# Optimization experiments

Measured on AMD Instinct MI355X. Metric: run time of the kernel, lower is better.

## Reference

```python
import jax, jax.numpy as jnp
import numpy as np

L, B, T, D = 4, 2, 1024, 2048
HQ, HKV, DK = 16, 4, 128
HID = 5464
CAND = 896


def setup_inputs() -> dict:
    key = jax.random.key(0)
    ks = jax.random.split(key, 8)
    s = lambda fan: fan ** -0.5
    return {
        "x": jax.random.normal(ks[0], (B, T, D), jnp.float32),
        "s1": jnp.ones((L, D), jnp.float32),
        "s2": jnp.ones((L, D), jnp.float32),
        "s3": jnp.ones((L, D), jnp.float32),
        "wq": jax.random.normal(ks[1], (L, D, HQ * DK), jnp.float32) * s(D),
        "wk": jax.random.normal(ks[2], (L, D, HKV * DK), jnp.float32) * s(D),
        "wv": jax.random.normal(ks[3], (L, D, HKV * DK), jnp.float32) * s(D),
        "wo": jax.random.normal(ks[4], (L, HQ * DK, D), jnp.float32) * s(HQ * DK),
        "w_gate": jax.random.normal(ks[5], (L, D, HID), jnp.float32) * s(D),
        "w_val": jax.random.normal(ks[6], (L, D, HID), jnp.float32) * s(D),
        "w_out": jax.random.normal(ks[7], (L, HID, D), jnp.float32) * s(HID),
        "cand_offset": CAND,
    }


def _rmsnorm(x, scale, eps=1e-5):
    xf = x.astype(jnp.float32)
    n = xf * jax.lax.rsqrt(jnp.mean(xf * xf, axis=-1, keepdims=True) + eps)
    return (scale * n).astype(x.dtype)


def _rope_cos_sin(t_len, dk):
    inv = 1.0 / (10000.0 ** (jnp.arange(0, dk, 2, dtype=jnp.float32) / dk))
    fr = jnp.outer(jnp.arange(t_len, dtype=jnp.float32), inv)
    emb = jnp.concatenate([fr, fr], axis=-1)  # [T, dk]
    return jnp.cos(emb)[None, :, None, :], jnp.sin(emb)[None, :, None, :]


def _rotate_half(x):
    x1, x2 = jnp.split(x, 2, axis=-1)
    return jnp.concatenate([-x2, x1], axis=-1)


def reference(x, s1, s2, s3, wq, wk, wv, wo, w_gate, w_val, w_out, cand_offset):
    Bsz, Tlen, _ = x.shape
    # recsys mask: causal history; candidates attend to history + self only
    r = jnp.arange(Tlen)[:, None]
    c = jnp.arange(Tlen)[None, :]
    mask = (c <= r) & ~((r >= cand_offset) & (c >= cand_offset) & (r != c))  # [T,T] bool
    cos, sin = _rope_cos_sin(Tlen, DK)
    nrep = HQ // HKV
    h = x
    for l in range(wq.shape[0]):
        hn = _rmsnorm(h, s1[l])
        q = (hn @ wq[l]).reshape(Bsz, Tlen, HQ, DK)
        k = (hn @ wk[l]).reshape(Bsz, Tlen, HKV, DK)
        v = (hn @ wv[l]).reshape(Bsz, Tlen, HKV, DK)
        q = q * cos + _rotate_half(q) * sin
        k = k * cos + _rotate_half(k) * sin
        k = jnp.repeat(k, nrep, axis=2)  # GQA expand -> [B,T,HQ,DK]
        v = jnp.repeat(v, nrep, axis=2)
        logits = jnp.einsum('bthd,bshd->bhts', q, k)  # attn_output_multiplier = 1.0
        logits = jnp.where(mask[None, None], logits, -jnp.inf)
        attn = jax.nn.softmax(logits.astype(jnp.float32), axis=-1).astype(x.dtype)
        o = jnp.einsum('bhts,bshd->bthd', attn, v).reshape(Bsz, Tlen, HQ * DK)
        h = h + o @ wo[l]
        hn = _rmsnorm(h, s2[l])
        ff = (jax.nn.gelu(hn @ w_gate[l], approximate=False) * (hn @ w_val[l])) @ w_out[l]
        h = h + ff
        h = _rmsnorm(h, s3[l])
    return h
```

## Files before the change

### kernel.cpp

```cpp
#include <hip/hip_runtime.h>
#include <stdint.h>

#define L_ 4
#define B_ 2
#define T_ 1024
#define D_ 2048
#define HQ_ 16
#define HKV_ 4
#define DK_ 128
#define HID_ 5464
#define HIDP_ 5504
#define BT_ (B_*T_)

typedef unsigned short u16;
typedef float f32x4 __attribute__((ext_vector_type(4)));
typedef __bf16 bf16x8 __attribute__((ext_vector_type(8)));

__device__ __forceinline__ u16 f2bs(float f) {
  unsigned u = __float_as_uint(f);
  u += 0x7fffu + ((u >> 16) & 1u);
  return (u16)(u >> 16);
}
__device__ __forceinline__ float bs2f(u16 s) {
  return __uint_as_float(((unsigned)s) << 16);
}

__device__ __forceinline__ void async16(void* lds, const void* g) {
  __builtin_amdgcn_global_load_lds(
      (const __attribute__((address_space(1))) unsigned*)(uintptr_t)g,
      (__attribute__((address_space(3))) unsigned*)(unsigned)(uintptr_t)lds,
      16, 0, 0);
}

__device__ __forceinline__ f32x4 mfma16(bf16x8 a, bf16x8 b, f32x4 c) {
  return __builtin_amdgcn_mfma_f32_16x16x32_bf16(a, b, c, 0, 0, 0);
}

__device__ __forceinline__ void remap_bid(int& bm, int& bn) {
  const int nbx = gridDim.x, nby = gridDim.y;
  const int nwg = nbx * nby;
  const int lin = blockIdx.y * nbx + blockIdx.x;
  const int q = nwg >> 3, r = nwg & 7;
  const int xcd = lin & 7, rest = lin >> 3;
  const int wgid = (xcd < r ? xcd * (q + 1) : r * (q + 1) + (xcd - r) * q) + rest;
  const int GROUP = 4;
  const int tpg = GROUP * nby;
  const int gid = wgid / tpg;
  const int first = gid * GROUP;
  const int size = (GROUP < nbx - first) ? GROUP : (nbx - first);
  const int rem = wgid - gid * tpg;
  bn = first + rem % size;
  bm = rem / size;
}

__global__ void copy_f4_k(const float4* __restrict__ src, float4* __restrict__ dst, int n4) {
  int i = blockIdx.x * blockDim.x + threadIdx.x;
  if (i < n4) dst[i] = src[i];
}

__global__ void rope_tab_k(float* __restrict__ ct, float* __restrict__ st) {
  int idx = blockIdx.x * 256 + threadIdx.x;
  int t = idx >> 6, i = idx & 63;
  float inv = expf(-(float)i * (9.210340371976184f / 64.f));
  float fr = (float)t * inv;
  ct[idx] = cosf(fr);
  st[idx] = sinf(fr);
}

__global__ __launch_bounds__(256) void cvt_split_k(const float4* __restrict__ in,
    uint2* __restrict__ ohi, uint2* __restrict__ olo, int n4) {
  int i = blockIdx.x * 256 + threadIdx.x;
  if (i >= n4) return;
  float4 v = in[i];
  u16 h0 = f2bs(v.x), h1 = f2bs(v.y), h2 = f2bs(v.z), h3 = f2bs(v.w);
  u16 l0 = f2bs(v.x - bs2f(h0)), l1 = f2bs(v.y - bs2f(h1));
  u16 l2 = f2bs(v.z - bs2f(h2)), l3 = f2bs(v.w - bs2f(h3));
  uint2 ph, pl;
  ph.x = (unsigned)h0 | ((unsigned)h1 << 16); ph.y = (unsigned)h2 | ((unsigned)h3 << 16);
  pl.x = (unsigned)l0 | ((unsigned)l1 << 16); pl.y = (unsigned)l2 | ((unsigned)l3 << 16);
  ohi[i] = ph; olo[i] = pl;
}

__global__ __launch_bounds__(256) void transpose_split_k(
    const float* __restrict__ in, u16* __restrict__ outh, u16* __restrict__ outl,
    int inR, int inC, int outC) {
  __shared__ float tile[64][65];
  const int oj0 = blockIdx.x * 64;
  const int oi0 = blockIdx.y * 64;
  #pragma unroll
  for (int rep = 0; rep < 16; ++rep) {
    int idx = rep * 256 + threadIdx.x;
    int a = idx >> 6, b = idx & 63;
    int ir = oj0 + a, ic = oi0 + b;
    tile[a][b] = (ir < inR && ic < inC) ? in[(size_t)ir * inC + ic] : 0.f;
  }
  __syncthreads();
  #pragma unroll
  for (int rep = 0; rep < 16; ++rep) {
    int idx = rep * 256 + threadIdx.x;
    int ii = idx >> 6, jj = idx & 63;
    float val = tile[jj][ii];
    u16 hh = f2bs(val);
    const size_t o = (size_t)(oi0 + ii) * outC + oj0 + jj;
    outh[o] = hh;
    outl[o] = f2bs(val - bs2f(hh));
  }
}

__global__ __launch_bounds__(256) void transpose_v_split_k(const float* __restrict__ v,
    u16* __restrict__ vth, u16* __restrict__ vtl) {
  __shared__ float tile[64][65];
  const int bz = blockIdx.z;
  const int b = bz >> 2, hkv = bz & 3;
  const int t0 = blockIdx.x * 64, d0 = blockIdx.y * 64;
  #pragma unroll
  for (int rep = 0; rep < 16; ++rep) {
    int idx = rep * 256 + threadIdx.x;
    int a = idx >> 6, c = idx & 63;
    tile[a][c] = v[((size_t)(b * T_ + t0 + a) * HKV_ + hkv) * DK_ + d0 + c];
  }
  __syncthreads();
  #pragma unroll
  for (int rep = 0; rep < 16; ++rep) {
    int idx = rep * 256 + threadIdx.x;
    int aa = idx & 63, cc = idx >> 6;
    float val = tile[aa][cc];
    u16 hh = f2bs(val);
    const size_t o = ((size_t)bz * DK_ + d0 + cc) * T_ + t0 + aa;
    vth[o] = hh;
    vtl[o] = f2bs(val - bs2f(hh));
  }
}

__global__ __launch_bounds__(256) void rmsnorm_f(const float* x,
    const float* __restrict__ sc, float* out) {
  const int row = blockIdx.x;
  const float* xr = x + (size_t)row * D_;
  float ss = 0.f;
  #pragma unroll
  for (int it = 0; it < D_ / 1024; ++it) {
    int i = (it * 256 + threadIdx.x) * 4;
    float4 v = *(const float4*)(xr + i);
    ss += v.x * v.x + v.y * v.y + v.z * v.z + v.w * v.w;
  }
  #pragma unroll
  for (int o = 1; o < 64; o <<= 1) ss += __shfl_xor(ss, o);
  __shared__ float red[4];
  if ((threadIdx.x & 63) == 0) red[threadIdx.x >> 6] = ss;
  __syncthreads();
  float tot = red[0] + red[1] + red[2] + red[3];
  float r = rsqrtf(tot * (1.f / D_) + 1e-5f);
  float* orow = out + (size_t)row * D_;
  #pragma unroll
  for (int it = 0; it < D_ / 1024; ++it) {
    int i = (it * 256 + threadIdx.x) * 4;
    float4 v = *(const float4*)(xr + i);
    float4 s4 = *(const float4*)(sc + i);
    float4 o4;
    o4.x = v.x * s4.x * r; o4.y = v.y * s4.y * r;
    o4.z = v.z * s4.z * r; o4.w = v.w * s4.w * r;
    *(float4*)(orow + i) = o4;
  }
}

__global__ __launch_bounds__(256) void rmsnorm_s(const float* x,
    const float* __restrict__ sc, u16* ohi, u16* olo) {
  const int row = blockIdx.x;
  const float* xr = x + (size_t)row * D_;
  float ss = 0.f;
  #pragma unroll
  for (int it = 0; it < D_ / 1024; ++it) {
    int i = (it * 256 + threadIdx.x) * 4;
    float4 v = *(const float4*)(xr + i);
    ss += v.x * v.x + v.y * v.y + v.z * v.z + v.w * v.w;
  }
  #pragma unroll
  for (int o = 1; o < 64; o <<= 1) ss += __shfl_xor(ss, o);
  __shared__ float red[4];
  if ((threadIdx.x & 63) == 0) red[threadIdx.x >> 6] = ss;
  __syncthreads();
  float tot = red[0] + red[1] + red[2] + red[3];
  float r = rsqrtf(tot * (1.f / D_) + 1e-5f);
  #pragma unroll
  for (int it = 0; it < D_ / 1024; ++it) {
    int i = (it * 256 + threadIdx.x) * 4;
    float4 v = *(const float4*)(xr + i);
    float4 s4 = *(const float4*)(sc + i);
    float o0 = v.x * s4.x * r, o1 = v.y * s4.y * r, o2 = v.z * s4.z * r, o3 = v.w * s4.w * r;
    u16 h0 = f2bs(o0), h1 = f2bs(o1), h2 = f2bs(o2), h3 = f2bs(o3);
    u16 l0 = f2bs(o0 - bs2f(h0)), l1 = f2bs(o1 - bs2f(h1));
    u16 l2 = f2bs(o2 - bs2f(h2)), l3 = f2bs(o3 - bs2f(h3));
    uint2 ph, pl;
    ph.x = (unsigned)h0 | ((unsigned)h1 << 16); ph.y = (unsigned)h2 | ((unsigned)h3 << 16);
    pl.x = (unsigned)l0 | ((unsigned)l1 << 16); pl.y = (unsigned)l2 | ((unsigned)l3 << 16);
    *(uint2*)(ohi + (size_t)row * D_ + i) = ph;
    *(uint2*)(olo + (size_t)row * D_ + i) = pl;
  }
}

template <int MODE>
__global__ __launch_bounds__(512, 4) void gemm_bts_k(
    const u16* __restrict__ Ahi, const u16* __restrict__ Alo,
    const u16* __restrict__ Bthi, const u16* __restrict__ Btlo,
    float* Cf, u16* Chi, u16* Clo, int N, int K) {
  __shared__ u16 smem[128 * 64 * 4];
  char* Ash = (char*)smem;
  char* Asl = (char*)smem + 16384;
  char* Bsh = (char*)smem + 32768;
  char* Bsl = (char*)smem + 49152;
  const int tid = threadIdx.x, w = tid >> 6, lane = tid & 63;
  const int g = lane >> 4, r16 = lane & 15;
  int bm, bn;
  remap_bid(bm, bn);
  const int m0 = bm * 128, n0 = bn * 128;
  const int wr = w >> 1, wc = w & 1;
  f32x4 acc[2][4] = {};
  const int nkt = K >> 6;
  for (int kt = 0; kt < nkt; ++kt) {
    #pragma unroll
    for (int inst = 0; inst < 2; ++inst) {
      const int p = (inst * 8 + w) * 1024 + lane * 16;
      const int row = p >> 7;
      const int sc = ((p >> 4) & 7) ^ (row & 7);
      const size_t ga = (size_t)(m0 + row) * K + (kt << 6) + sc * 8;
      const size_t gb = (size_t)(n0 + row) * K + (kt << 6) + sc * 8;
      async16(Ash + p, Ahi + ga);
      async16(Asl + p, Alo + ga);
      async16(Bsh + p, Bthi + gb);
      async16(Bsl + p, Btlo + gb);
    }
    asm volatile("s_waitcnt vmcnt(0)" ::: "memory");
    __syncthreads();
    #pragma unroll
    for (int ks = 0; ks < 2; ++ks) {
      bf16x8 ah[2], al[2], bh[4], bl[4];
      #pragma unroll
      for (int m = 0; m < 2; ++m) {
        const int row = wr * 32 + m * 16 + r16;
        const int ch = (ks * 4 + g) ^ (row & 7);
        const int off = row * 128 + ch * 16;
        ah[m] = *(const bf16x8*)(Ash + off);
        al[m] = *(const bf16x8*)(Asl + off);
      }
      #pragma unroll
      for (int n = 0; n < 4; ++n) {
        const int row = wc * 64 + n * 16 + r16;
        const int ch = (ks * 4 + g) ^ (row & 7);
        const int off = row * 128 + ch * 16;
        bh[n] = *(const bf16x8*)(Bsh + off);
        bl[n] = *(const bf16x8*)(Bsl + off);
      }
      #pragma unroll
      for (int m = 0; m < 2; ++m)
        #pragma unroll
        for (int n = 0; n < 4; ++n) {
          acc[m][n] = mfma16(ah[m], bh[n], acc[m][n]);
          acc[m][n] = mfma16(ah[m], bl[n], acc[m][n]);
          acc[m][n] = mfma16(al[m], bh[n], acc[m][n]);
        }
    }
    __syncthreads();
  }
  #pragma unroll
  for (int m = 0; m < 2; ++m) {
    const int rbase = m0 + wr * 32 + m * 16 + g * 4;
    #pragma unroll
    for (int n = 0; n < 4; ++n) {
      const int c = n0 + wc * 64 + n * 16 + r16;
      #pragma unroll
      for (int j = 0; j < 4; ++j) {
        const size_t idx = (size_t)(rbase + j) * N + c;
        const float v = acc[m][n][j];
        if constexpr (MODE == 0) {
          Cf[idx] = v;
        } else if constexpr (MODE == 1) {
          Cf[idx] += v;
        } else if constexpr (MODE == 2) {
          const float gv = bs2f(Chi[idx]) + bs2f(Clo[idx]);
          const float ge = 0.5f * gv * (1.f + erff(gv * 0.70710678118654752f));
          const float r = ge * v;
          const u16 rh = f2bs(r);
          Chi[idx] = rh;
          Clo[idx] = f2bs(r - bs2f(rh));
        } else {
          const u16 rh = f2bs(v);
          Chi[idx] = rh;
          Clo[idx] = f2bs(v - bs2f(rh));
        }
      }
    }
  }
}

__global__ __launch_bounds__(256) void rope_f_k(float* q, float* k,
    const float* __restrict__ ct, const float* __restrict__ st) {
  const int row = blockIdx.x;
  const int t = row & (T_ - 1);
  float* qr = q + (size_t)row * (HQ_ * DK_);
  for (int idx = threadIdx.x; idx < HQ_ * 64; idx += 256) {
    int h = idx >> 6, i = idx & 63;
    float c = ct[t * 64 + i], s = st[t * 64 + i];
    float x1 = qr[h * DK_ + i], x2 = qr[h * DK_ + i + 64];
    qr[h * DK_ + i]      = x1 * c - x2 * s;
    qr[h * DK_ + i + 64] = x2 * c + x1 * s;
  }
  float* kr = k + (size_t)row * (HKV_ * DK_);
  for (int idx = threadIdx.x; idx < HKV_ * 64; idx += 256) {
    int h = idx >> 6, i = idx & 63;
    float c = ct[t * 64 + i], s = st[t * 64 + i];
    float x1 = kr[h * DK_ + i], x2 = kr[h * DK_ + i + 64];
    kr[h * DK_ + i]      = x1 * c - x2 * s;
    kr[h * DK_ + i + 64] = x2 * c + x1 * s;
  }
}

__global__ __launch_bounds__(256) void attn_s_k(
    const u16* __restrict__ Qh, const u16* __restrict__ Ql,
    const u16* __restrict__ Kh, const u16* __restrict__ Kl,
    const u16* __restrict__ VTh, const u16* __restrict__ VTl,
    u16* __restrict__ Ohi, u16* __restrict__ Olo, const int* __restrict__ candp) {
  __shared__ u16 sm[40960];
  char* Kth = (char*)sm;
  char* Ktl = (char*)sm + 16384;
  char* Vth = (char*)sm + 32768;
  char* Vtl = (char*)sm + 49152;
  const int b = blockIdx.z, hq = blockIdx.y, q0 = blockIdx.x * 64;
  const int hkv = hq >> 2;
  const int tid = threadIdx.x, w = tid >> 6, lane = tid & 63;
  const int g = lane >> 4, r16 = lane & 15;
  char* Pth = (char*)sm + 65536 + w * 2048;
  char* Ptl = (char*)sm + 65536 + 8192 + w * 2048;
  const int CANDv = *candp;
  const int qrow = q0 + w * 16 + r16;
  const int pmask = (r16 & 7) << 4;
  const u16* qph = Qh + ((size_t)(b * T_ + qrow) * HQ_ + hq) * DK_;
  const u16* qpl = Ql + ((size_t)(b * T_ + qrow) * HQ_ + hq) * DK_;
  bf16x8 qh[4], ql[4];
  #pragma unroll
  for (int ks = 0; ks < 4; ++ks) {
    qh[ks] = *(const bf16x8*)(qph + ks * 32 + g * 8);
    ql[ks] = *(const bf16x8*)(qpl + ks * 32 + g * 8);
  }

  float m_run = -1e30f, l_run = 0.f;
  f32x4 oacc[8] = {};

  const int ntile = blockIdx.x + 1;
  for (int it = 0; it < ntile; ++it) {
    const int c0 = it * 64;
    if (c0 >= CANDv && c0 + 63 < q0) continue;
    #pragma unroll
    for (int inst = 0; inst < 4; ++inst) {
      const int p = (inst * 4 + w) * 1024 + lane * 16;
      const int rowK = p >> 8;
      const int scK = ((p >> 4) & 15) ^ (rowK & 7);
      const size_t gk = ((size_t)(b * T_ + c0 + rowK) * HKV_ + hkv) * DK_ + scK * 8;
      async16(Kth + p, Kh + gk);
      async16(Ktl + p, Kl + gk);
      const int rowV = p >> 7;
      const int scV = ((p >> 4) & 7) ^ (rowV & 7);
      const size_t gv = ((size_t)(b * HKV_ + hkv) * DK_ + rowV) * T_ + c0 + scV * 8;
      async16(Vth + p, VTh + gv);
      async16(Vtl + p, VTl + gv);
    }
    asm volatile("s_waitcnt vmcnt(0)" ::: "memory");
    __syncthreads();

    f32x4 stf[4] = {};
    #pragma unroll
    for (int ks = 0; ks < 4; ++ks) {
      #pragma unroll
      for (int kf = 0; kf < 4; ++kf) {
        const int row = kf * 16 + r16;
        const int ch = (ks * 4 + g) ^ (row & 7);
        const int off = row * 256 + ch * 16;
        bf16x8 akh = *(const bf16x8*)(Kth + off);
        bf16x8 akl = *(const bf16x8*)(Ktl + off);
        stf[kf] = mfma16(akh, qh[ks], stf[kf]);
        stf[kf] = mfma16(akh, ql[ks], stf[kf]);
        stf[kf] = mfma16(akl, qh[ks], stf[kf]);
      }
    }
    float pv[16];
    float tmax = -1e30f;
    #pragma unroll
    for (int kf = 0; kf < 4; ++kf)
      #pragma unroll
      for (int j = 0; j < 4; ++j) {
        const int c = c0 + kf * 16 + g * 4 + j;
        float s = stf[kf][j];
        const bool ok = (c <= qrow) && !((qrow >= CANDv) && (c >= CANDv) && (c != qrow));
        s = ok ? s : -1e30f;
        pv[kf * 4 + j] = s;
        tmax = fmaxf(tmax, s);
      }
    tmax = fmaxf(tmax, __shfl_xor(tmax, 16));
    tmax = fmaxf(tmax, __shfl_xor(tmax, 32));
    const float mnew = fmaxf(m_run, tmax);
    const float scal = __expf(m_run - mnew);
    float psum = 0.f;
    #pragma unroll
    for (int i = 0; i < 16; ++i) {
      const float e = (pv[i] > -1e29f) ? __expf(pv[i] - mnew) : 0.f;
      pv[i] = e; psum += e;
    }
    psum += __shfl_xor(psum, 16);
    psum += __shfl_xor(psum, 32);
    l_run = l_run * scal + psum;
    m_run = mnew;
    #pragma unroll
    for (int df = 0; df < 8; ++df)
      #pragma unroll
      for (int j = 0; j < 4; ++j) oacc[df][j] *= scal;
    #pragma unroll
    for (int kf = 0; kf < 4; ++kf) {
      u16 h0 = f2bs(pv[kf * 4 + 0]), h1 = f2bs(pv[kf * 4 + 1]);
      u16 h2 = f2bs(pv[kf * 4 + 2]), h3 = f2bs(pv[kf * 4 + 3]);
      u16 l0 = f2bs(pv[kf * 4 + 0] - bs2f(h0)), l1 = f2bs(pv[kf * 4 + 1] - bs2f(h1));
      u16 l2 = f2bs(pv[kf * 4 + 2] - bs2f(h2)), l3 = f2bs(pv[kf * 4 + 3] - bs2f(h3));
      uint2 ph, pl;
      ph.x = (unsigned)h0 | ((unsigned)h1 << 16); ph.y = (unsigned)h2 | ((unsigned)h3 << 16);
      pl.x = (unsigned)l0 | ((unsigned)l1 << 16); pl.y = (unsigned)l2 | ((unsigned)l3 << 16);
      *(uint2*)(Pth + r16 * 128 + ((kf * 32 + g * 8) ^ pmask)) = ph;
      *(uint2*)(Ptl + r16 * 128 + ((kf * 32 + g * 8) ^ pmask)) = pl;
    }
    asm volatile("s_waitcnt lgkmcnt(0)" ::: "memory");
    __builtin_amdgcn_sched_barrier(0);
    #pragma unroll
    for (int ks = 0; ks < 2; ++ks) {
      bf16x8 pfh = *(const bf16x8*)(Pth + r16 * 128 + ((ks * 64 + g * 16) ^ pmask));
      bf16x8 pfl = *(const bf16x8*)(Ptl + r16 * 128 + ((ks * 64 + g * 16) ^ pmask));
      #pragma unroll
      for (int df = 0; df < 8; ++df) {
        const int row = df * 16 + r16;
        const int ch = (ks * 4 + g) ^ (row & 7);
        const int off = row * 128 + ch * 16;
        bf16x8 avh = *(const bf16x8*)(Vth + off);
        bf16x8 avl = *(const bf16x8*)(Vtl + off);
        oacc[df] = mfma16(avh, pfh, oacc[df]);
        oacc[df] = mfma16(avh, pfl, oacc[df]);
        oacc[df] = mfma16(avl, pfh, oacc[df]);
      }
    }
    __syncthreads();
  }
  const float inv = 1.f / l_run;
  u16* oph = Ohi + ((size_t)(b * T_ + qrow) * HQ_ + hq) * DK_;
  u16* opl = Olo + ((size_t)(b * T_ + qrow) * HQ_ + hq) * DK_;
  #pragma unroll
  for (int df = 0; df < 8; ++df) {
    float o0 = oacc[df][0] * inv, o1 = oacc[df][1] * inv;
    float o2 = oacc[df][2] * inv, o3 = oacc[df][3] * inv;
    u16 h0 = f2bs(o0), h1 = f2bs(o1), h2 = f2bs(o2), h3 = f2bs(o3);
    u16 l0 = f2bs(o0 - bs2f(h0)), l1 = f2bs(o1 - bs2f(h1));
    u16 l2 = f2bs(o2 - bs2f(h2)), l3 = f2bs(o3 - bs2f(h3));
    uint2 ph, pl;
    ph.x = (unsigned)h0 | ((unsigned)h1 << 16); ph.y = (unsigned)h2 | ((unsigned)h3 << 16);
    pl.x = (unsigned)l0 | ((unsigned)l1 << 16); pl.y = (unsigned)l2 | ((unsigned)l3 << 16);
    *(uint2*)(oph + df * 16 + g * 4) = ph;
    *(uint2*)(opl + df * 16 + g * 4) = pl;
  }
}

extern "C" void kernel_launch(void* const* d_in, const int* in_sizes, int n_in,
                              void* d_out, int out_size, void* d_ws, size_t ws_size,
                              hipStream_t stream) {
  (void)in_sizes; (void)n_in; (void)out_size; (void)ws_size;
  const float* x    = (const float*)d_in[0];
  const float* s1   = (const float*)d_in[1];
  const float* s2   = (const float*)d_in[2];
  const float* s3   = (const float*)d_in[3];
  const float* wq   = (const float*)d_in[4];
  const float* wk   = (const float*)d_in[5];
  const float* wv   = (const float*)d_in[6];
  const float* wo   = (const float*)d_in[7];
  const float* wg   = (const float*)d_in[8];
  const float* wvl  = (const float*)d_in[9];
  const float* wout = (const float*)d_in[10];
  const int*   cand = (const int*)d_in[11];

  float* h = (float*)d_out;
  char* ws = (char*)d_ws;
  size_t off = 0;
  auto nxt = [&](size_t bytes) -> char* {
    char* p = ws + off; off += (bytes + 255) & ~(size_t)255; return p;
  };
  u16* wThi  = (u16*)nxt((size_t)HIDP_ * D_ * 2);
  u16* wTlo  = (u16*)nxt((size_t)HIDP_ * D_ * 2);
  u16* hnhi  = (u16*)nxt((size_t)BT_ * D_ * 2);
  u16* hnlo  = (u16*)nxt((size_t)BT_ * D_ * 2);
  char* U    = nxt((size_t)68 << 20);
  float* ct  = (float*)nxt((size_t)T_ * 64 * 4);
  float* st  = (float*)nxt((size_t)T_ * 64 * 4);
  size_t uo = 0;
  auto unxt = [&](size_t bytes) -> char* {
    char* p = U + uo; uo += (bytes + 255) & ~(size_t)255; return p;
  };
  float* qf   = (float*)unxt((size_t)BT_ * HQ_ * DK_ * 4);
  float* kf   = (float*)unxt((size_t)BT_ * HKV_ * DK_ * 4);
  float* vf   = (float*)unxt((size_t)BT_ * HKV_ * DK_ * 4);
  u16* qbhi   = (u16*)unxt((size_t)BT_ * HQ_ * DK_ * 2);
  u16* qblo   = (u16*)unxt((size_t)BT_ * HQ_ * DK_ * 2);
  u16* kbhi   = (u16*)unxt((size_t)BT_ * HKV_ * DK_ * 2);
  u16* kblo   = (u16*)unxt((size_t)BT_ * HKV_ * DK_ * 2);
  u16* vthi   = (u16*)unxt((size_t)BT_ * HKV_ * DK_ * 2);
  u16* vtlo   = (u16*)unxt((size_t)BT_ * HKV_ * DK_ * 2);
  u16* obhi   = (u16*)unxt((size_t)BT_ * HQ_ * DK_ * 2);
  u16* oblo   = (u16*)unxt((size_t)BT_ * HQ_ * DK_ * 2);
  u16* ghi = (u16*)U;
  u16* glo = (u16*)(U + (size_t)BT_ * HIDP_ * 2);

  copy_f4_k<<<BT_ * D_ / 4 / 256, 256, 0, stream>>>((const float4*)x, (float4*)h, BT_ * D_ / 4);
  rope_tab_k<<<T_ * 64 / 256, 256, 0, stream>>>(ct, st);

  for (int l = 0; l < L_; ++l) {
    const float* wq_l   = wq   + (size_t)l * D_ * (HQ_ * DK_);
    const float* wk_l   = wk   + (size_t)l * D_ * (HKV_ * DK_);
    const float* wv_l   = wv   + (size_t)l * D_ * (HKV_ * DK_);
    const float* wo_l   = wo   + (size_t)l * (HQ_ * DK_) * D_;
    const float* wg_l   = wg   + (size_t)l * D_ * HID_;
    const float* wvl_l  = wvl  + (size_t)l * D_ * HID_;
    const float* wout_l = wout + (size_t)l * HID_ * D_;

    rmsnorm_s<<<BT_, 256, 0, stream>>>(h, s1 + (size_t)l * D_, hnhi, hnlo);
    transpose_split_k<<<dim3(32, 32), 256, 0, stream>>>(wq_l, wThi, wTlo, D_, HQ_ * DK_, D_);
    transpose_split_k<<<dim3(32, 8), 256, 0, stream>>>(wk_l, wThi + (size_t)HQ_ * DK_ * D_,
        wTlo + (size_t)HQ_ * DK_ * D_, D_, HKV_ * DK_, D_);
    transpose_split_k<<<dim3(32, 8), 256, 0, stream>>>(wv_l, wThi + (size_t)(HQ_ + HKV_) * DK_ * D_,
        wTlo + (size_t)(HQ_ + HKV_) * DK_ * D_, D_, HKV_ * DK_, D_);
    gemm_bts_k<0><<<dim3(HQ_ * DK_ / 128, BT_ / 128), 512, 0, stream>>>(
        hnhi, hnlo, wThi, wTlo, qf, nullptr, nullptr, HQ_ * DK_, D_);
    gemm_bts_k<0><<<dim3(HKV_ * DK_ / 128, BT_ / 128), 512, 0, stream>>>(
        hnhi, hnlo, wThi + (size_t)HQ_ * DK_ * D_, wTlo + (size_t)HQ_ * DK_ * D_,
        kf, nullptr, nullptr, HKV_ * DK_, D_);
    gemm_bts_k<0><<<dim3(HKV_ * DK_ / 128, BT_ / 128), 512, 0, stream>>>(
        hnhi, hnlo, wThi + (size_t)(HQ_ + HKV_) * DK_ * D_, wTlo + (size_t)(HQ_ + HKV_) * DK_ * D_,
        vf, nullptr, nullptr, HKV_ * DK_, D_);
    rope_f_k<<<BT_, 256, 0, stream>>>(qf, kf, ct, st);
    cvt_split_k<<<BT_ * D_ / 4 / 256, 256, 0, stream>>>((const float4*)qf,
        (uint2*)qbhi, (uint2*)qblo, BT_ * D_ / 4);
    cvt_split_k<<<BT_ * HKV_ * DK_ / 4 / 256, 256, 0, stream>>>((const float4*)kf,
        (uint2*)kbhi, (uint2*)kblo, BT_ * HKV_ * DK_ / 4);
    transpose_v_split_k<<<dim3(T_ / 64, DK_ / 64, B_ * HKV_), 256, 0, stream>>>(vf, vthi, vtlo);
    attn_s_k<<<dim3(T_ / 64, HQ_, B_), 256, 0, stream>>>(
        qbhi, qblo, kbhi, kblo, vthi, vtlo, obhi, oblo, cand);
    transpose_split_k<<<dim3(32, 32), 256, 0, stream>>>(wo_l, wThi, wTlo, HQ_ * DK_, D_, D_);
    gemm_bts_k<1><<<dim3(D_ / 128, BT_ / 128), 512, 0, stream>>>(
        obhi, oblo, wThi, wTlo, h, nullptr, nullptr, D_, D_);

    rmsnorm_s<<<BT_, 256, 0, stream>>>(h, s2 + (size_t)l * D_, hnhi, hnlo);
    transpose_split_k<<<dim3(32, HIDP_ / 64), 256, 0, stream>>>(wg_l, wThi, wTlo, D_, HID_, D_);
    gemm_bts_k<3><<<dim3(HIDP_ / 128, BT_ / 128), 512, 0, stream>>>(
        hnhi, hnlo, wThi, wTlo, nullptr, ghi, glo, HIDP_, D_);
    transpose_split_k<<<dim3(32, HIDP_ / 64), 256, 0, stream>>>(wvl_l, wThi, wTlo, D_, HID_, D_);
    gemm_bts_k<2><<<dim3(HIDP_ / 128, BT_ / 128), 512, 0, stream>>>(
        hnhi, hnlo, wThi, wTlo, nullptr, ghi, glo, HIDP_, D_);
    transpose_split_k<<<dim3(HIDP_ / 64, 32), 256, 0, stream>>>(wout_l, wThi, wTlo, HID_, D_, HIDP_);
    gemm_bts_k<1><<<dim3(D_ / 128, BT_ / 128), 512, 0, stream>>>(
        ghi, glo, wThi, wTlo, h, nullptr, nullptr, D_, HIDP_);
    rmsnorm_f<<<BT_, 256, 0, stream>>>(h, s3 + (size_t)l * D_, h);
  }
}
```

Before: 3.663 ms.

## Double-buffer GEMM LDS tiles with BK=32 to overlap loads and MFMA

```diff
diff --git a/kernel.cpp b/kernel.cpp
--- a/kernel.cpp
+++ b/kernel.cpp
@@ -203,11 +203,7 @@
     const u16* __restrict__ Ahi, const u16* __restrict__ Alo,
     const u16* __restrict__ Bthi, const u16* __restrict__ Btlo,
     float* Cf, u16* Chi, u16* Clo, int N, int K) {
-  __shared__ u16 smem[128 * 64 * 4];
-  char* Ash = (char*)smem;
-  char* Asl = (char*)smem + 16384;
-  char* Bsh = (char*)smem + 32768;
-  char* Bsl = (char*)smem + 49152;
+  __shared__ u16 smem[128 * 32 * 4 * 2];
   const int tid = threadIdx.x, w = tid >> 6, lane = tid & 63;
   const int g = lane >> 4, r16 = lane & 15;
   int bm, bn;
@@ -215,51 +211,64 @@
   const int m0 = bm * 128, n0 = bn * 128;
   const int wr = w >> 1, wc = w & 1;
   f32x4 acc[2][4] = {};
-  const int nkt = K >> 6;
+  const int nkt = K >> 5;
+
+  const int sp = tid * 16;
+  const int srow = sp >> 6;
+  const int ssc = ((sp >> 4) & 3) ^ ((srow >> 1) & 3);
+  auto stage = [&](int kt, int buf) {
+    char* base = (char*)smem + buf * 32768;
+    const size_t ga = (size_t)(m0 + srow) * K + (kt << 5) + ssc * 8;
+    const size_t gb = (size_t)(n0 + srow) * K + (kt << 5) + ssc * 8;
+    async16(base + sp, Ahi + ga);
+    async16(base + 8192 + sp, Alo + ga);
+    async16(base + 16384 + sp, Bthi + gb);
+    async16(base + 24576 + sp, Btlo + gb);
+  };
+
+  stage(0, 0);
   for (int kt = 0; kt < nkt; ++kt) {
-    #pragma unroll
-    for (int inst = 0; inst < 2; ++inst) {
-      const int p = (inst * 8 + w) * 1024 + lane * 16;
-      const int row = p >> 7;
-      const int sc = ((p >> 4) & 7) ^ (row & 7);
-      const size_t ga = (size_t)(m0 + row) * K + (kt << 6) + sc * 8;
-      const size_t gb = (size_t)(n0 + row) * K + (kt << 6) + sc * 8;
-      async16(Ash + p, Ahi + ga);
-      async16(Asl + p, Alo + ga);
-      async16(Bsh + p, Bthi + gb);
-      async16(Bsl + p, Btlo + gb);
-    }
-    asm volatile("s_waitcnt vmcnt(0)" ::: "memory");
-    __syncthreads();
-    #pragma unroll
-    for (int ks = 0; ks < 2; ++ks) {
-      bf16x8 ah[2], al[2], bh[4], bl[4];
-      #pragma unroll
-      for (int m = 0; m < 2; ++m) {
-        const int row = wr * 32 + m * 16 + r16;
-        const int ch = (ks * 4 + g) ^ (row & 7);
-        const int off = row * 128 + ch * 16;
-        ah[m] = *(const bf16x8*)(Ash + off);
-        al[m] = *(const bf16x8*)(Asl + off);
-      }
+    const int cur = kt & 1;
+    if (kt + 1 < nkt) {
+      stage(kt + 1, cur ^ 1);
+      asm volatile("s_waitcnt vmcnt(4)" ::: "memory");
+    } else {
+      asm volatile("s_waitcnt vmcnt(0)" ::: "memory");
+    }
+    __builtin_amdgcn_s_barrier();
+    __builtin_amdgcn_sched_barrier(0);
+    char* Ash = (char*)smem + cur * 32768;
+    char* Asl = Ash + 8192;
+    char* Bsh = Ash + 16384;
+    char* Bsl = Ash + 24576;
+    bf16x8 ah[2], al[2], bh[4], bl[4];
+    #pragma unroll
+    for (int m = 0; m < 2; ++m) {
+      const int row = wr * 32 + m * 16 + r16;
+      const int ch = g ^ ((row >> 1) & 3);
+      const int off = row * 64 + ch * 16;
+      ah[m] = *(const bf16x8*)(Ash + off);
+      al[m] = *(const bf16x8*)(Asl + off);
+    }
+    #pragma unroll
+    for (int n = 0; n < 4; ++n) {
+      const int row = wc * 64 + n * 16 + r16;
+      const int ch = g ^ ((row >> 1) & 3);
+      const int off = row * 64 + ch * 16;
+      bh[n] = *(const bf16x8*)(Bsh + off);
+      bl[n] = *(const bf16x8*)(Bsl + off);
+    }
+    #pragma unroll
+    for (int m = 0; m < 2; ++m)
       #pragma unroll
       for (int n = 0; n < 4; ++n) {
-        const int row = wc * 64 + n * 16 + r16;
-        const int ch = (ks * 4 + g) ^ (row & 7);
-        const int off = row * 128 + ch * 16;
-        bh[n] = *(const bf16x8*)(Bsh + off);
-        bl[n] = *(const bf16x8*)(Bsl + off);
+        acc[m][n] = mfma16(ah[m], bh[n], acc[m][n]);
+        acc[m][n] = mfma16(ah[m], bl[n], acc[m][n]);
+        acc[m][n] = mfma16(al[m], bh[n], acc[m][n]);
       }
-      #pragma unroll
-      for (int m = 0; m < 2; ++m)
-        #pragma unroll
-        for (int n = 0; n < 4; ++n) {
-          acc[m][n] = mfma16(ah[m], bh[n], acc[m][n]);
-          acc[m][n] = mfma16(ah[m], bl[n], acc[m][n]);
-          acc[m][n] = mfma16(al[m], bh[n], acc[m][n]);
-        }
-    }
-    __syncthreads();
+    asm volatile("s_waitcnt lgkmcnt(0)" ::: "memory");
+    __builtin_amdgcn_s_barrier();
+    __builtin_amdgcn_sched_barrier(0);
   }
   #pragma unroll
   for (int m = 0; m < 2; ++m) {
```

New measurement: 3.429 ms. -6.4%, faster.
